# Performance work log

Hardware: AMD Instinct MI355X
Metric: run time of the kernel (lower is better)

## Reference

```python
import jax, jax.numpy as jnp
import numpy as np


def setup_inputs() -> dict:
    key = jax.random.key(0)
    k1, k2, k3 = jax.random.split(key, 3)
    B, C, N, G, D = 64, 4, 1024, 32, 3
    patches = jax.random.normal(k1, (B, C, N, G, D), dtype=jnp.float32)
    centers = jax.random.normal(k2, (B, C, N, D), dtype=jnp.float32)
    # crops_centers_idx: uniform multinomial over n_patches, one per flat batch elem
    center_idx = jax.random.randint(k3, (B * C,), 0, N)
    # crop_length ~ randint(0.25*N, 0.75*N); fixed to midpoint 512 for static shapes
    return {"patches": patches, "centers": centers, "center_idx": center_idx, "K": 512}


def reference(patches, centers, center_idx, K):
    B, C, N, G, D = patches.shape
    BF = B * C
    # flatten (b, c) -> bf, matching PatchedCloud.flatten()
    p = patches.reshape(BF, N, G, D)
    c = centers.reshape(BF, N, D)
    # gather the sampled crop center per flat batch element: [BF, D]
    q = c[jnp.arange(BF), center_idx]
    # knn_points: squared L2 distances from query to all centers, K smallest (sorted)
    d2 = jnp.sum((q[:, None, :] - c) ** 2, axis=-1)  # [BF, N]
    _, idx = jax.lax.top_k(-d2, K)                   # [BF, K], ascending distance
    b = jnp.arange(BF)[:, None]
    cropped_patches = p[b, idx]   # [BF, K, G, D]
    cropped_centers = c[b, idx]   # [BF, K, D]
    return (cropped_patches.reshape(B, C, K, G, D),
            cropped_centers.reshape(B, C, K, D))
```

## Files before the change

### kernel.cpp

```cpp
#include <hip/hip_runtime.h>
#include <hip/hip_bf16.h>

#define BFN   256
#define NPTS  1024
#define KSEL  512
#define GD    96
#define ROW4  24
#define PBLK  12288
#define CBLK  512

typedef unsigned long long u64;

__global__ __launch_bounds__(1024)
void sel_kernel(const float* __restrict__ centers,
                const int*   __restrict__ center_idx,
                int* __restrict__ out_idx)
{
    __shared__ u64 lds[NPTS];
    const int bf = blockIdx.x;
    const int t  = threadIdx.x;

    const float* cbase = centers + (size_t)bf * NPTS * 3;
    const int qi = center_idx[bf];
    const float q0 = cbase[qi * 3 + 0], q1 = cbase[qi * 3 + 1], q2 = cbase[qi * 3 + 2];
    const float c0 = cbase[t * 3 + 0],  c1 = cbase[t * 3 + 1],  c2 = cbase[t * 3 + 2];

    const double e0 = (double)q0 - (double)c0;
    const double e1 = (double)q1 - (double)c1;
    const double e2 = (double)q2 - (double)c2;
    const double d2 = e0 * e0 + e1 * e1 + e2 * e2;

    u64 key = (((u64)__double_as_longlong(d2)) & ~0x3FFull) | (u64)t;

    for (int size = 2; size <= NPTS; size <<= 1) {
        const bool dir = (t & size) != 0;
        for (int stride = size >> 1; stride > 0; stride >>= 1) {
            u64 other;
            if (stride >= 64) {
                __syncthreads();
                lds[t] = key;
                __syncthreads();
                other = lds[t ^ stride];
            } else {
                other = __shfl_xor(key, stride, 64);
            }
            const bool upper    = (t & stride) != 0;
            const bool keep_min = (upper == dir);
            const bool mine_lt  = key < other;
            key = (keep_min == mine_lt) ? key : other;
        }
    }

    if (t < KSEL) out_idx[bf * KSEL + t] = (int)(key & 0x3FFull);
}

__global__ __launch_bounds__(256)
void gather_kernel(const float* __restrict__ patches,
                   const float* __restrict__ centers,
                   const int*   __restrict__ idx,
                   float* __restrict__ out_p,
                   float* __restrict__ out_c)
{
    const int b = blockIdx.x;
    const int t = threadIdx.x;
    if (b < PBLK) {
        const int i    = b * 256 + t;
        const int row  = i / ROW4;
        const int lane = i - row * ROW4;
        const int bf   = row >> 9;
        const int src  = idx[row];
        const float4* pb = (const float4*)patches;
        float4 v = pb[((size_t)bf * NPTS + src) * ROW4 + lane];
        ((float4*)out_p)[(size_t)row * ROW4 + lane] = v;
    } else {
        const int r  = (b - PBLK) * 256 + t;
        const int bf = r >> 9;
        const int src = idx[r];
        const float* cb = centers + ((size_t)bf * NPTS + src) * 3;
        float* oc = out_c + (size_t)r * 3;
        oc[0] = cb[0]; oc[1] = cb[1]; oc[2] = cb[2];
    }
}

extern "C" void kernel_launch(void* const* d_in, const int* in_sizes, int n_in,
                              void* d_out, int out_size, void* d_ws, size_t ws_size,
                              hipStream_t stream)
{
    const float* patches    = (const float*)d_in[0];
    const float* centers    = (const float*)d_in[1];
    const int*   center_idx = (const int*)d_in[2];

    float* out_patches = (float*)d_out;
    float* out_centers = (float*)d_out + (size_t)BFN * KSEL * GD;
    int*   idx_ws      = (int*)d_ws;

    sel_kernel<<<BFN, 1024, 0, stream>>>(centers, center_idx, idx_ws);
    gather_kernel<<<PBLK + CBLK, 256, 0, stream>>>(patches, centers, idx_ws,
                                                   out_patches, out_centers);
}
```

Measured before the change: 167.7 us.

## Invert gather to streaming reads with rank-based scattered writes

The selection kernel now writes a per-point rank map (−1 for unselected points) and gathers the selected centers itself. The patch kernel then streams every source row contiguously and scatters only the selected rows to their ranked output positions. The aim is to replace random row reads with sequential reads and to remove a separate centers pass. In exchange it reads all patches, including the unselected half, and uses fewer, longer-running blocks.

```diff
diff --git a/kernel.cpp b/kernel.cpp
--- a/kernel.cpp
+++ b/kernel.cpp
@@ -6,19 +6,20 @@
 #define KSEL  512
 #define GD    96
 #define ROW4  24
-#define PBLK  12288
-#define CBLK  512
 
 typedef unsigned long long u64;
 
 __global__ __launch_bounds__(1024)
 void sel_kernel(const float* __restrict__ centers,
                 const int*   __restrict__ center_idx,
-                int* __restrict__ out_idx)
+                int* __restrict__ rank_ws,
+                float* __restrict__ out_centers)
 {
     __shared__ u64 lds[NPTS];
     const int bf = blockIdx.x;
     const int t  = threadIdx.x;
+
+    rank_ws[bf * NPTS + t] = -1;
 
     const float* cbase = centers + (size_t)bf * NPTS * 3;
     const int qi = center_idx[bf];
@@ -50,35 +51,42 @@
             key = (keep_min == mine_lt) ? key : other;
         }
     }
+    __syncthreads();
 
-    if (t < KSEL) out_idx[bf * KSEL + t] = (int)(key & 0x3FFull);
+    if (t < KSEL) {
+        const int idx = (int)(key & 0x3FFull);
+        rank_ws[bf * NPTS + idx] = t;
+        const float* cs = cbase + (size_t)idx * 3;
+        float* oc = out_centers + ((size_t)bf * KSEL + t) * 3;
+        oc[0] = cs[0]; oc[1] = cs[1]; oc[2] = cs[2];
+    }
 }
 
 __global__ __launch_bounds__(256)
-void gather_kernel(const float* __restrict__ patches,
-                   const float* __restrict__ centers,
-                   const int*   __restrict__ idx,
-                   float* __restrict__ out_p,
-                   float* __restrict__ out_c)
+void gather_kernel(const float4* __restrict__ patches4,
+                   const int*    __restrict__ rank_ws,
+                   float4*       __restrict__ out_p4)
 {
-    const int b = blockIdx.x;
-    const int t = threadIdx.x;
-    if (b < PBLK) {
-        const int i    = b * 256 + t;
-        const int row  = i / ROW4;
-        const int lane = i - row * ROW4;
-        const int bf   = row >> 9;
-        const int src  = idx[row];
-        const float4* pb = (const float4*)patches;
-        float4 v = pb[((size_t)bf * NPTS + src) * ROW4 + lane];
-        ((float4*)out_p)[(size_t)row * ROW4 + lane] = v;
-    } else {
-        const int r  = (b - PBLK) * 256 + t;
-        const int bf = r >> 9;
-        const int src = idx[r];
-        const float* cb = centers + ((size_t)bf * NPTS + src) * 3;
-        float* oc = out_c + (size_t)r * 3;
-        oc[0] = cb[0]; oc[1] = cb[1]; oc[2] = cb[2];
+    __shared__ int rank_s[256];
+    const int b     = blockIdx.x;
+    const int bf    = b >> 2;
+    const int chunk = b & 3;
+    const int t     = threadIdx.x;
+
+    rank_s[t] = rank_ws[bf * NPTS + chunk * 256 + t];
+    __syncthreads();
+
+    const float4* src = patches4 + ((size_t)bf * NPTS + (size_t)chunk * 256) * ROW4;
+    float4*       dst = out_p4   + (size_t)bf * KSEL * ROW4;
+
+    #pragma unroll
+    for (int it = 0; it < 24; ++it) {
+        const int flat = it * 256 + t;
+        const float4 v = src[flat];
+        const int row  = flat / 24;
+        const int lane = flat - row * 24;
+        const int r    = rank_s[row];
+        if (r >= 0) dst[(size_t)r * ROW4 + lane] = v;
     }
 }
 
@@ -92,9 +100,9 @@
 
     float* out_patches = (float*)d_out;
     float* out_centers = (float*)d_out + (size_t)BFN * KSEL * GD;
-    int*   idx_ws      = (int*)d_ws;
+    int*   rank_ws     = (int*)d_ws;
 
-    sel_kernel<<<BFN, 1024, 0, stream>>>(centers, center_idx, idx_ws);
-    gather_kernel<<<PBLK + CBLK, 256, 0, stream>>>(patches, centers, idx_ws,
-                                                   out_patches, out_centers);
+    sel_kernel<<<BFN, 1024, 0, stream>>>(centers, center_idx, rank_ws, out_centers);
+    gather_kernel<<<BFN * 4, 256, 0, stream>>>((const float4*)patches, rank_ws,
+                                               (float4*)out_patches);
 }
```

New measurement: 170.4 us. No clear change (+1.6%).
